# Kernel tuning notes

Hardware: AMD Instinct MI355X
Metric: run time of the kernel (lower is better)

Reference implementation:

```python
import jax, jax.numpy as jnp
import numpy as np

H = 32  # node_hidden_size
B = 16  # number of graphs in the batch


def setup_inputs() -> dict:
    key = jax.random.key(0)
    ks = iter(jax.random.split(key, 32))
    N, E = 20000, 200000
    rn = lambda s, scale=0.1: jax.random.normal(next(ks), s, dtype=jnp.float32) * scale
    return {
        "x": jax.random.normal(next(ks), (N, 4), dtype=jnp.float32),
        "edge_index": jax.random.randint(next(ks), (2, E), 0, N),
        "edge_attr": jax.random.normal(next(ks), (E,), dtype=jnp.float32),
        "batch": jnp.sort(jax.random.randint(next(ks), (N,), 0, B)),
        # project: Linear(4,32)
        "proj_w": rn((4, H)), "proj_b": jnp.zeros((H,), jnp.float32),
        # edge_nn: Linear(1,8) -> ReLU -> Linear(8,32*32)
        "e1_w": rn((1, 8)), "e1_b": jnp.zeros((8,), jnp.float32),
        "e2_w": rn((8, H * H)), "e2_b": jnp.zeros((H * H,), jnp.float32),
        # NNConv root weight + bias
        "root_w": rn((H, H)), "conv_b": jnp.zeros((H,), jnp.float32),
        # GRU(32,32), torch layout [3H, in]/[3H, H], gate order r,z,n
        "gru_wi": rn((3 * H, H)), "gru_wh": rn((3 * H, H)),
        "gru_bi": jnp.zeros((3 * H,), jnp.float32), "gru_bh": jnp.zeros((3 * H,), jnp.float32),
        # Set2Set LSTM(2H -> H), gate order i,f,g,o
        "lstm_wi": rn((4 * H, 2 * H)), "lstm_wh": rn((4 * H, H)),
        "lstm_bi": jnp.zeros((4 * H,), jnp.float32), "lstm_bh": jnp.zeros((4 * H,), jnp.float32),
        # FFN: 2H -> H -> H -> 1 (dropout is identity at inference)
        "f1_w": rn((2 * H, H)), "f1_b": jnp.zeros((H,), jnp.float32),
        "f2_w": rn((H, H)), "f2_b": jnp.zeros((H,), jnp.float32),
        "f3_w": rn((H, 1)), "f3_b": jnp.zeros((1,), jnp.float32),
    }


def reference(x, edge_index, edge_attr, batch,
              proj_w, proj_b, e1_w, e1_b, e2_w, e2_b, root_w, conv_b,
              gru_wi, gru_wh, gru_bi, gru_bh,
              lstm_wi, lstm_wh, lstm_bi, lstm_bh,
              f1_w, f1_b, f2_w, f2_b, f3_w, f3_b):
    N = x.shape[0]
    src, dst = edge_index[0], edge_index[1]

    # project node features
    h = jax.nn.relu(x @ proj_w + proj_b)              # [N, H]
    msg = h                                           # GRU hidden state

    # edge-conditioned weights (edge_attr unsqueezed to [E,1]); constant over steps
    ea = edge_attr[:, None]
    ew = (jax.nn.relu(ea @ e1_w + e1_b) @ e2_w + e2_b).reshape(-1, H, H)  # [E, in, out]

    for _ in range(3):  # message passing steps
        m = jnp.einsum('ei,eio->eo', h[src], ew)                  # per-edge matvec [E, H]
        agg = jax.ops.segment_sum(m, dst, num_segments=N)         # scatter-add to targets
        out = jax.nn.relu(agg + h @ root_w + conv_b)              # NNConv root + bias, then ReLU
        # GRU cell (seq_len=1)
        gi = out @ gru_wi.T + gru_bi
        gh = msg @ gru_wh.T + gru_bh
        r = jax.nn.sigmoid(gi[:, :H] + gh[:, :H])
        z = jax.nn.sigmoid(gi[:, H:2 * H] + gh[:, H:2 * H])
        n = jnp.tanh(gi[:, 2 * H:] + r * gh[:, 2 * H:])
        h = (1.0 - z) * n + z * msg
        msg = h

    # Set2Set readout, processing_steps=1
    q_star = jnp.zeros((B, 2 * H), x.dtype)
    hL = jnp.zeros((B, H), x.dtype)
    cL = jnp.zeros((B, H), x.dtype)
    g = q_star @ lstm_wi.T + lstm_bi + hL @ lstm_wh.T + lstm_bh   # [B, 4H]
    i_g = jax.nn.sigmoid(g[:, :H])
    f_g = jax.nn.sigmoid(g[:, H:2 * H])
    g_g = jnp.tanh(g[:, 2 * H:3 * H])
    o_g = jax.nn.sigmoid(g[:, 3 * H:])
    cL = f_g * cL + i_g * g_g
    q = o_g * jnp.tanh(cL)                                        # [B, H]
    # per-graph softmax attention
    e = jnp.sum(h * q[batch], axis=-1)                            # [N]
    e_max = jax.ops.segment_max(e, batch, num_segments=B)
    a = jnp.exp(e - e_max[batch])
    a = a / jax.ops.segment_sum(a, batch, num_segments=B)[batch]
    r_out = jax.ops.segment_sum(a[:, None] * h, batch, num_segments=B)  # [B, H]
    q_star = jnp.concatenate([q, r_out], axis=-1)                 # [B, 2H]

    # FFN (dropout = identity at inference)
    out = jax.nn.relu(q_star @ f1_w + f1_b)
    out = jax.nn.relu(out @ f2_w + f2_b)
    return out @ f3_w + f3_b                                      # [B, 1]
```

## Files before the change

kernel.cpp:

```cpp
#include <hip/hip_runtime.h>
#include <math.h>

#define H 32
#define BSEG 16
#define CHUNKS 32

__device__ __forceinline__ float sigmoidf_(float x){ return 1.f/(1.f+expf(-x)); }

__global__ __launch_bounds__(512) void k_prep(
    const float* __restrict__ gru_wi, const float* __restrict__ gru_wh,
    const float* __restrict__ gru_bi, const float* __restrict__ gru_bh,
    const float* __restrict__ lstm_bi, const float* __restrict__ lstm_bh,
    const float* __restrict__ e1w, const float* __restrict__ e1b, const float* __restrict__ e2w,
    float* __restrict__ WI, float* __restrict__ WH, float* __restrict__ BS,
    float* __restrict__ MP, float* __restrict__ MM, int* __restrict__ flag,
    float* __restrict__ qvec, unsigned int* __restrict__ segmax,
    float* __restrict__ ssum, float* __restrict__ vsum,
    int* __restrict__ cnt, int N)
{
    int t = threadIdx.x;
    for (int i = t; i < N; i += 512) cnt[i] = 0;
    for (int idx = t; idx < 3072; idx += 512) {
        int k = idx >> 10, rem = idx & 1023, i = rem >> 5, o = rem & 31;
        WI[idx] = gru_wi[(k*32 + o)*32 + i];
        WH[idx] = gru_wh[(k*32 + o)*32 + i];
    }
    for (int idx = t; idx < 1024; idx += 512) {
        float mp = 0.f, mm = 0.f;
        #pragma unroll
        for (int k = 0; k < 8; ++k) {
            float w = e1w[k];
            float v = e2w[k*1024 + idx];
            if (w > 0.f) mp = fmaf(w, v, mp);
            if (w < 0.f) mm = fmaf(w, v, mm);
        }
        MP[idx] = mp;
        MM[idx] = mm;
    }
    if (t == 0) {
        int z = 1;
        for (int k = 0; k < 8; ++k) if (e1b[k] != 0.f) z = 0;
        flag[0] = z;
    }
    if (t < 32) {
        BS[t]      = gru_bi[t]      + gru_bh[t];
        BS[32 + t] = gru_bi[32 + t] + gru_bh[32 + t];
        BS[64 + t] = gru_bi[64 + t];
        BS[96 + t] = gru_bh[64 + t];
    }
    if (t < H) {
        float g0 = lstm_bi[t] + lstm_bh[t];
        float g2 = lstm_bi[2*H + t] + lstm_bh[2*H + t];
        float g3 = lstm_bi[3*H + t] + lstm_bh[3*H + t];
        float ig = sigmoidf_(g0);
        float gg = tanhf(g2);
        float og = sigmoidf_(g3);
        qvec[t] = og * tanhf(ig * gg);
    }
    for (int i = t; i < BSEG; i += 512) { segmax[i] = 0u; ssum[i] = 0.f; }
    for (int i = t; i < BSEG*H; i += 512) vsum[i] = 0.f;
}

__global__ __launch_bounds__(256) void k_count(const int* __restrict__ ei, int* __restrict__ cnt, int E)
{
    int e = blockIdx.x * 256 + threadIdx.x;
    if (e < E) atomicAdd(&cnt[ei[E + e]], 1);
}

__global__ __launch_bounds__(1024) void k_scan(
    const int* __restrict__ cnt, int* __restrict__ rowptr, int* __restrict__ cursor, int N)
{
    __shared__ int part[1024];
    int t = threadIdx.x;
    int chunk = (N + 1023) >> 10;
    int base = t * chunk;
    int s = 0;
    for (int i = 0; i < chunk; ++i) {
        int idx = base + i;
        if (idx < N) s += cnt[idx];
    }
    part[t] = s;
    __syncthreads();
    for (int off = 1; off < 1024; off <<= 1) {
        int add = (t >= off) ? part[t - off] : 0;
        __syncthreads();
        part[t] += add;
        __syncthreads();
    }
    int run = part[t] - s;
    for (int i = 0; i < chunk; ++i) {
        int idx = base + i;
        if (idx < N) {
            rowptr[idx] = run;
            cursor[idx] = run;
            run += cnt[idx];
        }
    }
    if (t == 1023) rowptr[N] = part[1023];
}

__global__ __launch_bounds__(256) void k_scatter(
    const int* __restrict__ ei, const float* __restrict__ ea, int* __restrict__ cursor,
    int* __restrict__ esrc, float* __restrict__ eattr, int E)
{
    int e = blockIdx.x * 256 + threadIdx.x;
    if (e >= E) return;
    int dst = ei[E + e];
    int pos = atomicAdd(&cursor[dst], 1);
    esrc[pos] = ei[e];
    eattr[pos] = ea[e];
}

__device__ __forceinline__ void pass2_lds(const float* sm, int xb, int w0, int w1, int fg4,
                                          float a[4], float b[4])
{
    #pragma unroll 2
    for (int i4 = 0; i4 < 32; i4 += 4) {
        float4 xv  = *(const float4*)&sm[xb + i4];
        float4 w00 = *(const float4*)&sm[w0 + (i4+0)*32 + fg4];
        float4 w01 = *(const float4*)&sm[w0 + (i4+1)*32 + fg4];
        float4 w02 = *(const float4*)&sm[w0 + (i4+2)*32 + fg4];
        float4 w03 = *(const float4*)&sm[w0 + (i4+3)*32 + fg4];
        float4 w10 = *(const float4*)&sm[w1 + (i4+0)*32 + fg4];
        float4 w11 = *(const float4*)&sm[w1 + (i4+1)*32 + fg4];
        float4 w12 = *(const float4*)&sm[w1 + (i4+2)*32 + fg4];
        float4 w13 = *(const float4*)&sm[w1 + (i4+3)*32 + fg4];
        a[0]=fmaf(xv.x,w00.x,a[0]); a[1]=fmaf(xv.x,w00.y,a[1]); a[2]=fmaf(xv.x,w00.z,a[2]); a[3]=fmaf(xv.x,w00.w,a[3]);
        a[0]=fmaf(xv.y,w01.x,a[0]); a[1]=fmaf(xv.y,w01.y,a[1]); a[2]=fmaf(xv.y,w01.z,a[2]); a[3]=fmaf(xv.y,w01.w,a[3]);
        a[0]=fmaf(xv.z,w02.x,a[0]); a[1]=fmaf(xv.z,w02.y,a[1]); a[2]=fmaf(xv.z,w02.z,a[2]); a[3]=fmaf(xv.z,w02.w,a[3]);
        a[0]=fmaf(xv.w,w03.x,a[0]); a[1]=fmaf(xv.w,w03.y,a[1]); a[2]=fmaf(xv.w,w03.z,a[2]); a[3]=fmaf(xv.w,w03.w,a[3]);
        b[0]=fmaf(xv.x,w10.x,b[0]); b[1]=fmaf(xv.x,w10.y,b[1]); b[2]=fmaf(xv.x,w10.z,b[2]); b[3]=fmaf(xv.x,w10.w,b[3]);
        b[0]=fmaf(xv.y,w11.x,b[0]); b[1]=fmaf(xv.y,w11.y,b[1]); b[2]=fmaf(xv.y,w11.z,b[2]); b[3]=fmaf(xv.y,w11.w,b[3]);
        b[0]=fmaf(xv.z,w12.x,b[0]); b[1]=fmaf(xv.z,w12.y,b[1]); b[2]=fmaf(xv.z,w12.z,b[2]); b[3]=fmaf(xv.z,w12.w,b[3]);
        b[0]=fmaf(xv.w,w13.x,b[0]); b[1]=fmaf(xv.w,w13.y,b[1]); b[2]=fmaf(xv.w,w13.z,b[2]); b[3]=fmaf(xv.w,w13.w,b[3]);
    }
}

__device__ __forceinline__ void pass1_lds(const float* sm, int xb, int w0, int fg4, float a[4])
{
    #pragma unroll 2
    for (int i4 = 0; i4 < 32; i4 += 4) {
        float4 xv  = *(const float4*)&sm[xb + i4];
        float4 w00 = *(const float4*)&sm[w0 + (i4+0)*32 + fg4];
        float4 w01 = *(const float4*)&sm[w0 + (i4+1)*32 + fg4];
        float4 w02 = *(const float4*)&sm[w0 + (i4+2)*32 + fg4];
        float4 w03 = *(const float4*)&sm[w0 + (i4+3)*32 + fg4];
        a[0]=fmaf(xv.x,w00.x,a[0]); a[1]=fmaf(xv.x,w00.y,a[1]); a[2]=fmaf(xv.x,w00.z,a[2]); a[3]=fmaf(xv.x,w00.w,a[3]);
        a[0]=fmaf(xv.y,w01.x,a[0]); a[1]=fmaf(xv.y,w01.y,a[1]); a[2]=fmaf(xv.y,w01.z,a[2]); a[3]=fmaf(xv.y,w01.w,a[3]);
        a[0]=fmaf(xv.z,w02.x,a[0]); a[1]=fmaf(xv.z,w02.y,a[1]); a[2]=fmaf(xv.z,w02.z,a[2]); a[3]=fmaf(xv.z,w02.w,a[3]);
        a[0]=fmaf(xv.w,w03.x,a[0]); a[1]=fmaf(xv.w,w03.y,a[1]); a[2]=fmaf(xv.w,w03.z,a[2]); a[3]=fmaf(xv.w,w03.w,a[3]);
    }
}

__global__ __launch_bounds__(256) void k_proj(
    const float* __restrict__ x, const float* __restrict__ proj_w, const float* __restrict__ proj_b,
    float* __restrict__ h, int N)
{
    int n = blockIdx.x * 256 + threadIdx.x;
    if (n >= N) return;
    float4 xv = *(const float4*)&x[n * 4];
    #pragma unroll
    for (int q = 0; q < 8; ++q) {
        float r_[4];
        #pragma unroll
        for (int j = 0; j < 4; ++j) {
            int o = q*4 + j;
            float a = proj_b[o];
            a = fmaf(xv.x, proj_w[0*32 + o], a);
            a = fmaf(xv.y, proj_w[1*32 + o], a);
            a = fmaf(xv.z, proj_w[2*32 + o], a);
            a = fmaf(xv.w, proj_w[3*32 + o], a);
            r_[j] = fmaxf(a, 0.f);
        }
        *(float4*)&h[n*32 + q*4] = make_float4(r_[0], r_[1], r_[2], r_[3]);
    }
}

#define TW 3072
__global__ __launch_bounds__(256, 2) void k_tab(
    const float* __restrict__ h, const float* __restrict__ e2w, const float* __restrict__ e2b,
    const float* __restrict__ MP, const float* __restrict__ MM, const int* __restrict__ flag,
    float* __restrict__ A, int N)
{
    __shared__ float sm[TW + 4*288];
    int tid = threadIdx.x;
    int lane = tid & 63;
    int w = tid >> 6;
    int fg = lane & 7, fg4 = fg*4;
    int nw = lane >> 3;
    int n = (blockIdx.x * 4 + w) * 8 + nw;
    bool valid = (n < N);
    int nc = valid ? n : (N - 1);
    int xb = TW + w*288 + nw*36;

    float4 hv4 = *(const float4*)&h[nc*32 + fg4];
    *(float4*)&sm[xb + fg4] = hv4;

    if (flag[0]) {
        float4* s4 = (float4*)sm;
        for (int i = tid; i < 768; i += 256) {
            const float4* src = (i < 256) ? (const float4*)MP
                              : (i < 512) ? (const float4*)MM
                                          : (const float4*)e2b;
            s4[i] = src[i & 255];
        }
        __syncthreads();
        #pragma unroll 1
        for (int cc = 0; cc < 3; ++cc) {
            float acc[4] = {0.f, 0.f, 0.f, 0.f};
            pass1_lds(sm, xb, cc*1024, fg4, acc);
            if (valid)
                *(float4*)&A[(size_t)n*96 + cc*32 + fg4] =
                    make_float4(acc[0], acc[1], acc[2], acc[3]);
        }
    } else {
        #pragma unroll 1
        for (int cg = 0; cg < 3; ++cg) {
            __syncthreads();
            float4* s4 = (float4*)sm;
            for (int i = tid; i < 768; i += 256) {
                int c = cg*3 + (i >> 8);
                const float4* src = (c < 8) ? (const float4*)(e2w + (size_t)c*1024)
                                            : (const float4*)e2b;
                s4[i] = src[i & 255];
            }
            __syncthreads();
            #pragma unroll 1
            for (int cc = 0; cc < 3; ++cc) {
                float acc[4] = {0.f, 0.f, 0.f, 0.f};
                pass1_lds(sm, xb, cc*1024, fg4, acc);
                if (valid)
                    *(float4*)&A[(size_t)n*288 + (cg*3+cc)*32 + fg4] =
                        make_float4(acc[0], acc[1], acc[2], acc[3]);
            }
        }
    }
}

#define XGR 10240
__global__ __launch_bounds__(256, 2) void k_gru(
    float* __restrict__ h,
    const int* __restrict__ rowptr, const int* __restrict__ esrc, const float* __restrict__ eattr,
    const float* __restrict__ TIN, const int* __restrict__ flag,
    const float* __restrict__ root_w, const float* __restrict__ conv_b,
    const float* __restrict__ WI, const float* __restrict__ WH, const float* __restrict__ BS,
    const float* __restrict__ MP, const float* __restrict__ MM,
    const float* __restrict__ e2b, const float* __restrict__ e2w,
    const float* __restrict__ e1w, const float* __restrict__ e1b,
    float* __restrict__ TOUT, int N, int computeT)
{
    __shared__ float sm[XGR + 4*288];
    int tid = threadIdx.x;
    int fast = flag[0];
    {
        float4* s4 = (float4*)sm;
        const float4* r4  = (const float4*)root_w;
        const float4* wh4 = (const float4*)WH;
        const float4* wi4 = (const float4*)WI;
        for (int i = tid; i < 256; i += 256) s4[i] = r4[i];
        for (int i = tid; i < 768; i += 256) s4[256  + i] = wh4[i];
        for (int i = tid; i < 768; i += 256) s4[1024 + i] = wi4[i];
        if (computeT && fast) {
            for (int i = tid; i < 768; i += 256) {
                const float4* src = (i < 256) ? (const float4*)MP
                                  : (i < 512) ? (const float4*)MM
                                              : (const float4*)e2b;
                s4[1792 + i] = src[i & 255];
            }
        }
    }
    __syncthreads();

    int lane = tid & 63;
    int w = tid >> 6;
    int fg = lane & 7, fg4 = fg*4;
    int nw = lane >> 3;
    int n = (blockIdx.x * 4 + w) * 8 + nw;
    bool valid = (n < N);
    int nc = valid ? n : (N - 1);
    int xb = XGR + w*288 + nw*36;

    float4 hv4 = *(const float4*)&h[nc*32 + fg4];
    float hold[4] = {hv4.x, hv4.y, hv4.z, hv4.w};
    *(float4*)&sm[xb + fg4] = hv4;

    float av[4] = {0.f, 0.f, 0.f, 0.f};
    {
        int beg = rowptr[nc];
        int end = rowptr[nc + 1];
        if (fast) {
            for (int j = beg; j < end; ++j) {
                int src = esrc[j];
                float a = eattr[j];
                const float* base = TIN + (size_t)src * 96;
                float4 p = *(const float4*)&base[(a > 0.f ? 0 : 32) + fg4];
                float4 b = *(const float4*)&base[64 + fg4];
                av[0] += fmaf(a, p.x, b.x);
                av[1] += fmaf(a, p.y, b.y);
                av[2] += fmaf(a, p.z, b.z);
                av[3] += fmaf(a, p.w, b.w);
            }
        } else {
            for (int j = beg; j < end; ++j) {
                int src = esrc[j];
                float a = eattr[j];
                const float* Gp = TIN + (size_t)src * 288;
                float4 b = *(const float4*)&Gp[256 + fg4];
                float m0 = b.x, m1 = b.y, m2 = b.z, m3 = b.w;
                #pragma unroll
                for (int k = 0; k < 8; ++k) {
                    float t = fmaxf(fmaf(a, e1w[k], e1b[k]), 0.f);
                    float4 g = *(const float4*)&Gp[k*32 + fg4];
                    m0 = fmaf(t, g.x, m0); m1 = fmaf(t, g.y, m1);
                    m2 = fmaf(t, g.z, m2); m3 = fmaf(t, g.w, m3);
                }
                av[0] += m0; av[1] += m1; av[2] += m2; av[3] += m3;
            }
        }
    }

    float outv[4], gh2[4];
    {
        float4 cb4 = *(const float4*)&conv_b[fg4];
        outv[0]=av[0]+cb4.x; outv[1]=av[1]+cb4.y; outv[2]=av[2]+cb4.z; outv[3]=av[3]+cb4.w;
        float4 b3 = *(const float4*)&BS[96 + fg4];
        gh2[0]=b3.x; gh2[1]=b3.y; gh2[2]=b3.z; gh2[3]=b3.w;
    }
    pass2_lds(sm, xb, 0, 1024 + 2048, fg4, outv, gh2);

    float gh0[4] = {0.f,0.f,0.f,0.f};
    float gh1[4] = {0.f,0.f,0.f,0.f};
    pass2_lds(sm, xb, 1024, 2048, fg4, gh0, gh1);

    float outr[4];
    #pragma unroll
    for (int j = 0; j < 4; ++j) outr[j] = fmaxf(outv[j], 0.f);

    *(float4*)&sm[xb + fg4] = make_float4(outr[0], outr[1], outr[2], outr[3]);

    float gi0[4], gi1[4], gi2[4];
    {
        float4 b0 = *(const float4*)&BS[fg4];
        float4 b1 = *(const float4*)&BS[32 + fg4];
        float4 b2 = *(const float4*)&BS[64 + fg4];
        gi0[0]=b0.x; gi0[1]=b0.y; gi0[2]=b0.z; gi0[3]=b0.w;
        gi1[0]=b1.x; gi1[1]=b1.y; gi1[2]=b1.z; gi1[3]=b1.w;
        gi2[0]=b2.x; gi2[1]=b2.y; gi2[2]=b2.z; gi2[3]=b2.w;
    }
    pass2_lds(sm, xb, 4096, 5120, fg4, gi0, gi1);
    pass1_lds(sm, xb, 6144, fg4, gi2);

    float hnew[4];
    #pragma unroll
    for (int j = 0; j < 4; ++j) {
        float r = sigmoidf_(gi0[j] + gh0[j]);
        float z = sigmoidf_(gi1[j] + gh1[j]);
        float nn = tanhf(gi2[j] + r * gh2[j]);
        hnew[j] = (1.f - z) * nn + z * hold[j];
    }
    if (valid) *(float4*)&h[n*32 + fg4] = make_float4(hnew[0], hnew[1], hnew[2], hnew[3]);

    if (computeT) {
        *(float4*)&sm[xb + fg4] = make_float4(hnew[0], hnew[1], hnew[2], hnew[3]);
        if (fast) {
            #pragma unroll 1
            for (int cc = 0; cc < 3; ++cc) {
                float acc[4] = {0.f, 0.f, 0.f, 0.f};
                pass1_lds(sm, xb, 7168 + cc*1024, fg4, acc);
                if (valid)
                    *(float4*)&TOUT[(size_t)n*96 + cc*32 + fg4] =
                        make_float4(acc[0], acc[1], acc[2], acc[3]);
            }
        } else {
            #pragma unroll 1
            for (int cg = 0; cg < 3; ++cg) {
                __syncthreads();
                float4* s4 = (float4*)sm;
                for (int i = tid; i < 768; i += 256) {
                    int c = cg*3 + (i >> 8);
                    const float4* src = (c < 8) ? (const float4*)(e2w + (size_t)c*1024)
                                                : (const float4*)e2b;
                    s4[1792 + i] = src[i & 255];
                }
                __syncthreads();
                #pragma unroll 1
                for (int cc = 0; cc < 3; ++cc) {
                    float acc[4] = {0.f, 0.f, 0.f, 0.f};
                    pass1_lds(sm, xb, 7168 + cc*1024, fg4, acc);
                    if (valid)
                        *(float4*)&TOUT[(size_t)n*288 + (cg*3+cc)*32 + fg4] =
                            make_float4(acc[0], acc[1], acc[2], acc[3]);
                }
            }
        }
    }
}

__device__ __forceinline__ unsigned int fenc(float f) {
    int i = __float_as_int(f);
    return (i >= 0) ? ((unsigned int)i | 0x80000000u) : ~(unsigned int)i;
}
__device__ __forceinline__ float fdec(unsigned int u) {
    int i = (u & 0x80000000u) ? (int)(u & 0x7FFFFFFFu) : (int)(~u);
    return __int_as_float(i);
}

__global__ __launch_bounds__(256) void k_pass1(
    const float* __restrict__ h, const int* __restrict__ batch,
    const float* __restrict__ qvec, float* __restrict__ ebuf,
    unsigned int* __restrict__ segmax, int N)
{
    int b = blockIdx.x / CHUNKS;
    int c = blockIdx.x % CHUNKS;
    int lo = 0, hi = N;
    while (lo < hi) { int mid = (lo + hi) >> 1; if (batch[mid] < b) lo = mid + 1; else hi = mid; }
    int s = lo;
    lo = 0; hi = N;
    while (lo < hi) { int mid = (lo + hi) >> 1; if (batch[mid] < b + 1) lo = mid + 1; else hi = mid; }
    int e = lo;
    int len = e - s;
    int per = (len + CHUNKS - 1) / CHUNKS;
    int n0 = s + c * per;
    int n1 = min(n0 + per, e);

    int tid = threadIdx.x;
    int ln = tid >> 5, o = tid & 31;
    float qv = qvec[o];
    float mloc = -INFINITY;
    for (int nn = n0 + ln; nn < n1; nn += 8) {
        float v = h[nn * H + o] * qv;
        #pragma unroll
        for (int m = 16; m >= 1; m >>= 1) v += __shfl_xor(v, m);
        if (o == 0) ebuf[nn] = v;
        mloc = fmaxf(mloc, v);
    }
    __shared__ float red[256];
    red[tid] = mloc;
    __syncthreads();
    for (int st = 128; st >= 1; st >>= 1) {
        if (tid < st) red[tid] = fmaxf(red[tid], red[tid + st]);
        __syncthreads();
    }
    if (tid == 0 && n0 < n1) atomicMax(&segmax[b], fenc(red[0]));
}

__global__ __launch_bounds__(256) void k_pass2(
    const float* __restrict__ h, const int* __restrict__ batch,
    const float* __restrict__ ebuf, const unsigned int* __restrict__ segmax,
    float* __restrict__ ssum, float* __restrict__ vsum, int N)
{
    int b = blockIdx.x / CHUNKS;
    int c = blockIdx.x % CHUNKS;
    int lo = 0, hi = N;
    while (lo < hi) { int mid = (lo + hi) >> 1; if (batch[mid] < b) lo = mid + 1; else hi = mid; }
    int s = lo;
    lo = 0; hi = N;
    while (lo < hi) { int mid = (lo + hi) >> 1; if (batch[mid] < b + 1) lo = mid + 1; else hi = mid; }
    int e = lo;
    int len = e - s;
    int per = (len + CHUNKS - 1) / CHUNKS;
    int n0 = s + c * per;
    int n1 = min(n0 + per, e);

    int tid = threadIdx.x;
    int ln = tid >> 5, o = tid & 31;
    float emax = fdec(segmax[b]);
    float vacc = 0.f, sacc = 0.f;
    for (int nn = n0 + ln; nn < n1; nn += 8) {
        float a = expf(ebuf[nn] - emax);
        vacc += a * h[nn * H + o];
        if (o == 0) sacc += a;
    }
    __shared__ float vsh[8][H];
    __shared__ float ssh[8];
    vsh[ln][o] = vacc;
    if (o == 0) ssh[ln] = sacc;
    __syncthreads();
    if (tid < H) {
        float v = 0.f;
        #pragma unroll
        for (int g = 0; g < 8; ++g) v += vsh[g][tid];
        atomicAdd(&vsum[b * H + tid], v);
    } else if (tid == H) {
        float stot = 0.f;
        #pragma unroll
        for (int g = 0; g < 8; ++g) stot += ssh[g];
        atomicAdd(&ssum[b], stot);
    }
}

__global__ __launch_bounds__(512) void k_mlp(
    const float* __restrict__ qvec, const float* __restrict__ ssum, const float* __restrict__ vsum,
    const float* __restrict__ f1w, const float* __restrict__ f1b,
    const float* __restrict__ f2w, const float* __restrict__ f2b,
    const float* __restrict__ f3w, const float* __restrict__ f3b,
    float* __restrict__ out)
{
    __shared__ float qsm[BSEG][2 * H];
    __shared__ float o1[BSEG][H];
    __shared__ float o2[BSEG][H];
    int tid = threadIdx.x;
    int b = tid >> 5, j = tid & 31;
    float st = ssum[b];
    qsm[b][j] = qvec[j];
    qsm[b][H + j] = (st > 0.f) ? vsum[b * H + j] / st : 0.f;
    __syncthreads();
    float acc = f1b[j];
    for (int i = 0; i < 2 * H; ++i) acc += qsm[b][i] * f1w[i * H + j];
    o1[b][j] = fmaxf(acc, 0.f);
    __syncthreads();
    acc = f2b[j];
    for (int i = 0; i < H; ++i) acc += o1[b][i] * f2w[i * H + j];
    o2[b][j] = fmaxf(acc, 0.f);
    __syncthreads();
    float v = o2[b][j] * f3w[j];
    #pragma unroll
    for (int m = 16; m >= 1; m >>= 1) v += __shfl_xor(v, m);
    if (j == 0) out[b] = v + f3b[0];
}

extern "C" void kernel_launch(void* const* d_in, const int* in_sizes, int n_in,
                              void* d_out, int out_size, void* d_ws, size_t ws_size,
                              hipStream_t stream)
{
    const float* x      = (const float*)d_in[0];
    const int*   ei     = (const int*)d_in[1];
    const float* ea     = (const float*)d_in[2];
    const int*   batch  = (const int*)d_in[3];
    const float* proj_w = (const float*)d_in[4];
    const float* proj_b = (const float*)d_in[5];
    const float* e1w    = (const float*)d_in[6];
    const float* e1b    = (const float*)d_in[7];
    const float* e2w    = (const float*)d_in[8];
    const float* e2b    = (const float*)d_in[9];
    const float* root_w = (const float*)d_in[10];
    const float* conv_b = (const float*)d_in[11];
    const float* gru_wi = (const float*)d_in[12];
    const float* gru_wh = (const float*)d_in[13];
    const float* gru_bi = (const float*)d_in[14];
    const float* gru_bh = (const float*)d_in[15];
    const float* lstm_bi = (const float*)d_in[18];
    const float* lstm_bh = (const float*)d_in[19];
    const float* f1w    = (const float*)d_in[20];
    const float* f1b    = (const float*)d_in[21];
    const float* f2w    = (const float*)d_in[22];
    const float* f2b    = (const float*)d_in[23];
    const float* f3w    = (const float*)d_in[24];
    const float* f3b    = (const float*)d_in[25];

    const int N = in_sizes[0] / 4;
    const int E = in_sizes[2];

    float* ws   = (float*)d_ws;
    float* h    = ws;
    float* A    = h + (size_t)N * H;
    float* Bb   = A + (size_t)N * 288;
    float* ebuf = Bb + (size_t)N * 288;
    float* qvec = ebuf + N;
    unsigned int* segmax = (unsigned int*)(qvec + H);
    float* ssum = (float*)(segmax + BSEG);
    float* vsum = ssum + BSEG;
    float* WI   = vsum + BSEG * H;
    float* WH   = WI + 3072;
    float* BS   = WH + 3072;
    float* MP   = BS + 128;
    float* MM   = MP + 1024;
    int*   flag = (int*)(MM + 1024);
    int*   cnt    = flag + 1;
    int*   rowptr = cnt + N;
    int*   cursor = rowptr + N + 1;
    int*   esrc   = cursor + N;
    float* eattr  = (float*)(esrc + E);

    const int nwaves = (N + 7) / 8;
    const int nb4 = (nwaves + 3) / 4;
    const int pblocks = (N + 255) / 256;
    const int cblocks = (E + 255) / 256;

    k_prep<<<1, 512, 0, stream>>>(gru_wi, gru_wh, gru_bi, gru_bh, lstm_bi, lstm_bh,
                                  e1w, e1b, e2w,
                                  WI, WH, BS, MP, MM, flag, qvec, segmax, ssum, vsum, cnt, N);
    k_count<<<cblocks, 256, 0, stream>>>(ei, cnt, E);
    k_scan<<<1, 1024, 0, stream>>>(cnt, rowptr, cursor, N);
    k_scatter<<<cblocks, 256, 0, stream>>>(ei, ea, cursor, esrc, eattr, E);
    k_proj<<<pblocks, 256, 0, stream>>>(x, proj_w, proj_b, h, N);
    k_tab<<<nb4, 256, 0, stream>>>(h, e2w, e2b, MP, MM, flag, A, N);

    k_gru<<<nb4, 256, 0, stream>>>(h, rowptr, esrc, eattr, A, flag, root_w, conv_b,
                                   WI, WH, BS, MP, MM, e2b, e2w, e1w, e1b, Bb, N, 1);
    k_gru<<<nb4, 256, 0, stream>>>(h, rowptr, esrc, eattr, Bb, flag, root_w, conv_b,
                                   WI, WH, BS, MP, MM, e2b, e2w, e1w, e1b, A, N, 1);
    k_gru<<<nb4, 256, 0, stream>>>(h, rowptr, esrc, eattr, A, flag, root_w, conv_b,
                                   WI, WH, BS, MP, MM, e2b, e2w, e1w, e1b, Bb, N, 0);

    k_pass1<<<BSEG * CHUNKS, 256, 0, stream>>>(h, batch, qvec, ebuf, segmax, N);
    k_pass2<<<BSEG * CHUNKS, 256, 0, stream>>>(h, batch, ebuf, segmax, ssum, vsum, N);
    k_mlp<<<1, 512, 0, stream>>>(qvec, ssum, vsum, f1w, f1b, f2w, f2b, f3w, f3b, (float*)d_out);
}
```

Baseline: 191.1 us.

## Split edge aggregation into wave-per-node kernel, fuse projection and attention scores

Moves the per-node edge gather out of the GRU kernel into a new kernel where each 64-lane wave handles one node, with 8 slots striding over its incoming edges and a shuffle reduction at the end. Previously 8 lanes walked each node's edge list serially, which left degree-dependent latency inside the heavy GRU kernel. The node projection is folded into the table kernel, and the final GRU step now computes attention logits and the per-segment max, so the separate projection and pass1 kernels are removed. In exchange it adds three extra launches and an N×32 intermediate buffer that is written and read back each step.

```diff
diff --git a/kernel.cpp b/kernel.cpp
--- a/kernel.cpp
+++ b/kernel.cpp
@@ -6,6 +6,15 @@
 #define CHUNKS 32
 
 __device__ __forceinline__ float sigmoidf_(float x){ return 1.f/(1.f+expf(-x)); }
+
+__device__ __forceinline__ unsigned int fenc(float f) {
+    int i = __float_as_int(f);
+    return (i >= 0) ? ((unsigned int)i | 0x80000000u) : ~(unsigned int)i;
+}
+__device__ __forceinline__ float fdec(unsigned int u) {
+    int i = (u & 0x80000000u) ? (int)(u & 0x7FFFFFFFu) : (int)(~u);
+    return __int_as_float(i);
+}
 
 __global__ __launch_bounds__(512) void k_prep(
     const float* __restrict__ gru_wi, const float* __restrict__ gru_wh,
@@ -152,35 +161,12 @@
     }
 }
 
-__global__ __launch_bounds__(256) void k_proj(
-    const float* __restrict__ x, const float* __restrict__ proj_w, const float* __restrict__ proj_b,
-    float* __restrict__ h, int N)
-{
-    int n = blockIdx.x * 256 + threadIdx.x;
-    if (n >= N) return;
-    float4 xv = *(const float4*)&x[n * 4];
-    #pragma unroll
-    for (int q = 0; q < 8; ++q) {
-        float r_[4];
-        #pragma unroll
-        for (int j = 0; j < 4; ++j) {
-            int o = q*4 + j;
-            float a = proj_b[o];
-            a = fmaf(xv.x, proj_w[0*32 + o], a);
-            a = fmaf(xv.y, proj_w[1*32 + o], a);
-            a = fmaf(xv.z, proj_w[2*32 + o], a);
-            a = fmaf(xv.w, proj_w[3*32 + o], a);
-            r_[j] = fmaxf(a, 0.f);
-        }
-        *(float4*)&h[n*32 + q*4] = make_float4(r_[0], r_[1], r_[2], r_[3]);
-    }
-}
-
 #define TW 3072
 __global__ __launch_bounds__(256, 2) void k_tab(
-    const float* __restrict__ h, const float* __restrict__ e2w, const float* __restrict__ e2b,
+    const float* __restrict__ x, const float* __restrict__ proj_w, const float* __restrict__ proj_b,
+    const float* __restrict__ e2w, const float* __restrict__ e2b,
     const float* __restrict__ MP, const float* __restrict__ MM, const int* __restrict__ flag,
-    float* __restrict__ A, int N)
+    float* __restrict__ h, float* __restrict__ A, int N)
 {
     __shared__ float sm[TW + 4*288];
     int tid = threadIdx.x;
@@ -193,8 +179,22 @@
     int nc = valid ? n : (N - 1);
     int xb = TW + w*288 + nw*36;
 
-    float4 hv4 = *(const float4*)&h[nc*32 + fg4];
-    *(float4*)&sm[xb + fg4] = hv4;
+    {
+        float4 xv = *(const float4*)&x[nc*4];
+        float r_[4];
+        #pragma unroll
+        for (int j = 0; j < 4; ++j) {
+            int o = fg4 + j;
+            float a = proj_b[o];
+            a = fmaf(xv.x, proj_w[0*32 + o], a);
+            a = fmaf(xv.y, proj_w[1*32 + o], a);
+            a = fmaf(xv.z, proj_w[2*32 + o], a);
+            a = fmaf(xv.w, proj_w[3*32 + o], a);
+            r_[j] = fmaxf(a, 0.f);
+        }
+        if (valid) *(float4*)&h[n*32 + fg4] = make_float4(r_[0], r_[1], r_[2], r_[3]);
+        *(float4*)&sm[xb + fg4] = make_float4(r_[0], r_[1], r_[2], r_[3]);
+    }
 
     if (flag[0]) {
         float4* s4 = (float4*)sm;
@@ -237,17 +237,71 @@
     }
 }
 
+__global__ __launch_bounds__(256) void k_agg(
+    const int* __restrict__ rowptr, const int* __restrict__ esrc, const float* __restrict__ eattr,
+    const float* __restrict__ T, const int* __restrict__ flag,
+    const float* __restrict__ e1w, const float* __restrict__ e1b,
+    float* __restrict__ agg, int N)
+{
+    int n = blockIdx.x * 4 + (threadIdx.x >> 6);
+    if (n >= N) return;
+    int lane = threadIdx.x & 63;
+    int slot = lane >> 3;
+    int fg4 = (lane & 7) * 4;
+    int beg = rowptr[n];
+    int end = rowptr[n + 1];
+
+    float a0 = 0.f, a1 = 0.f, a2 = 0.f, a3 = 0.f;
+    if (flag[0]) {
+        for (int j = beg + slot; j < end; j += 8) {
+            int src = esrc[j];
+            float a = eattr[j];
+            const float* base = T + (size_t)src * 96;
+            float4 p = *(const float4*)&base[(a > 0.f ? 0 : 32) + fg4];
+            float4 b = *(const float4*)&base[64 + fg4];
+            a0 += fmaf(a, p.x, b.x);
+            a1 += fmaf(a, p.y, b.y);
+            a2 += fmaf(a, p.z, b.z);
+            a3 += fmaf(a, p.w, b.w);
+        }
+    } else {
+        for (int j = beg + slot; j < end; j += 8) {
+            int src = esrc[j];
+            float a = eattr[j];
+            const float* Gp = T + (size_t)src * 288;
+            float4 b = *(const float4*)&Gp[256 + fg4];
+            float m0 = b.x, m1 = b.y, m2 = b.z, m3 = b.w;
+            #pragma unroll
+            for (int k = 0; k < 8; ++k) {
+                float t = fmaxf(fmaf(a, e1w[k], e1b[k]), 0.f);
+                float4 g = *(const float4*)&Gp[k*32 + fg4];
+                m0 = fmaf(t, g.x, m0); m1 = fmaf(t, g.y, m1);
+                m2 = fmaf(t, g.z, m2); m3 = fmaf(t, g.w, m3);
+            }
+            a0 += m0; a1 += m1; a2 += m2; a3 += m3;
+        }
+    }
+    #pragma unroll
+    for (int m = 8; m <= 32; m <<= 1) {
+        a0 += __shfl_xor(a0, m, 64);
+        a1 += __shfl_xor(a1, m, 64);
+        a2 += __shfl_xor(a2, m, 64);
+        a3 += __shfl_xor(a3, m, 64);
+    }
+    if (slot == 0)
+        *(float4*)&agg[(size_t)n*32 + fg4] = make_float4(a0, a1, a2, a3);
+}
+
 #define XGR 10240
 __global__ __launch_bounds__(256, 2) void k_gru(
-    float* __restrict__ h,
-    const int* __restrict__ rowptr, const int* __restrict__ esrc, const float* __restrict__ eattr,
-    const float* __restrict__ TIN, const int* __restrict__ flag,
+    float* __restrict__ h, const float* __restrict__ agg, const int* __restrict__ flag,
     const float* __restrict__ root_w, const float* __restrict__ conv_b,
     const float* __restrict__ WI, const float* __restrict__ WH, const float* __restrict__ BS,
     const float* __restrict__ MP, const float* __restrict__ MM,
     const float* __restrict__ e2b, const float* __restrict__ e2w,
-    const float* __restrict__ e1w, const float* __restrict__ e1b,
-    float* __restrict__ TOUT, int N, int computeT)
+    const float* __restrict__ qvec, const int* __restrict__ batch,
+    float* __restrict__ ebuf, unsigned int* __restrict__ segmax,
+    float* __restrict__ TOUT, int N, int computeT, int computeE)
 {
     __shared__ float sm[XGR + 4*288];
     int tid = threadIdx.x;
@@ -284,45 +338,11 @@
     float hold[4] = {hv4.x, hv4.y, hv4.z, hv4.w};
     *(float4*)&sm[xb + fg4] = hv4;
 
-    float av[4] = {0.f, 0.f, 0.f, 0.f};
-    {
-        int beg = rowptr[nc];
-        int end = rowptr[nc + 1];
-        if (fast) {
-            for (int j = beg; j < end; ++j) {
-                int src = esrc[j];
-                float a = eattr[j];
-                const float* base = TIN + (size_t)src * 96;
-                float4 p = *(const float4*)&base[(a > 0.f ? 0 : 32) + fg4];
-                float4 b = *(const float4*)&base[64 + fg4];
-                av[0] += fmaf(a, p.x, b.x);
-                av[1] += fmaf(a, p.y, b.y);
-                av[2] += fmaf(a, p.z, b.z);
-                av[3] += fmaf(a, p.w, b.w);
-            }
-        } else {
-            for (int j = beg; j < end; ++j) {
-                int src = esrc[j];
-                float a = eattr[j];
-                const float* Gp = TIN + (size_t)src * 288;
-                float4 b = *(const float4*)&Gp[256 + fg4];
-                float m0 = b.x, m1 = b.y, m2 = b.z, m3 = b.w;
-                #pragma unroll
-                for (int k = 0; k < 8; ++k) {
-                    float t = fmaxf(fmaf(a, e1w[k], e1b[k]), 0.f);
-                    float4 g = *(const float4*)&Gp[k*32 + fg4];
-                    m0 = fmaf(t, g.x, m0); m1 = fmaf(t, g.y, m1);
-                    m2 = fmaf(t, g.z, m2); m3 = fmaf(t, g.w, m3);
-                }
-                av[0] += m0; av[1] += m1; av[2] += m2; av[3] += m3;
-            }
-        }
-    }
-
     float outv[4], gh2[4];
     {
+        float4 av4 = *(const float4*)&agg[(size_t)nc*32 + fg4];
         float4 cb4 = *(const float4*)&conv_b[fg4];
-        outv[0]=av[0]+cb4.x; outv[1]=av[1]+cb4.y; outv[2]=av[2]+cb4.z; outv[3]=av[3]+cb4.w;
+        outv[0]=av4.x+cb4.x; outv[1]=av4.y+cb4.y; outv[2]=av4.z+cb4.z; outv[3]=av4.w+cb4.w;
         float4 b3 = *(const float4*)&BS[96 + fg4];
         gh2[0]=b3.x; gh2[1]=b3.y; gh2[2]=b3.z; gh2[3]=b3.w;
     }
@@ -359,6 +379,18 @@
         hnew[j] = (1.f - z) * nn + z * hold[j];
     }
     if (valid) *(float4*)&h[n*32 + fg4] = make_float4(hnew[0], hnew[1], hnew[2], hnew[3]);
+
+    if (computeE) {
+        float4 qv = *(const float4*)&qvec[fg4];
+        float e = hnew[0]*qv.x + hnew[1]*qv.y + hnew[2]*qv.z + hnew[3]*qv.w;
+        e += __shfl_xor(e, 1, 64);
+        e += __shfl_xor(e, 2, 64);
+        e += __shfl_xor(e, 4, 64);
+        if (valid && fg == 0) {
+            ebuf[n] = e;
+            atomicMax(&segmax[batch[n]], fenc(e));
+        }
+    }
 
     if (computeT) {
         *(float4*)&sm[xb + fg4] = make_float4(hnew[0], hnew[1], hnew[2], hnew[3]);
@@ -396,54 +428,6 @@
     }
 }
 
-__device__ __forceinline__ unsigned int fenc(float f) {
-    int i = __float_as_int(f);
-    return (i >= 0) ? ((unsigned int)i | 0x80000000u) : ~(unsigned int)i;
-}
-__device__ __forceinline__ float fdec(unsigned int u) {
-    int i = (u & 0x80000000u) ? (int)(u & 0x7FFFFFFFu) : (int)(~u);
-    return __int_as_float(i);
-}
-
-__global__ __launch_bounds__(256) void k_pass1(
-    const float* __restrict__ h, const int* __restrict__ batch,
-    const float* __restrict__ qvec, float* __restrict__ ebuf,
-    unsigned int* __restrict__ segmax, int N)
-{
-    int b = blockIdx.x / CHUNKS;
-    int c = blockIdx.x % CHUNKS;
-    int lo = 0, hi = N;
-    while (lo < hi) { int mid = (lo + hi) >> 1; if (batch[mid] < b) lo = mid + 1; else hi = mid; }
-    int s = lo;
-    lo = 0; hi = N;
-    while (lo < hi) { int mid = (lo + hi) >> 1; if (batch[mid] < b + 1) lo = mid + 1; else hi = mid; }
-    int e = lo;
-    int len = e - s;
-    int per = (len + CHUNKS - 1) / CHUNKS;
-    int n0 = s + c * per;
-    int n1 = min(n0 + per, e);
-
-    int tid = threadIdx.x;
-    int ln = tid >> 5, o = tid & 31;
-    float qv = qvec[o];
-    float mloc = -INFINITY;
-    for (int nn = n0 + ln; nn < n1; nn += 8) {
-        float v = h[nn * H + o] * qv;
-        #pragma unroll
-        for (int m = 16; m >= 1; m >>= 1) v += __shfl_xor(v, m);
-        if (o == 0) ebuf[nn] = v;
-        mloc = fmaxf(mloc, v);
-    }
-    __shared__ float red[256];
-    red[tid] = mloc;
-    __syncthreads();
-    for (int st = 128; st >= 1; st >>= 1) {
-        if (tid < st) red[tid] = fmaxf(red[tid], red[tid + st]);
-        __syncthreads();
-    }
-    if (tid == 0 && n0 < n1) atomicMax(&segmax[b], fenc(red[0]));
-}
-
 __global__ __launch_bounds__(256) void k_pass2(
     const float* __restrict__ h, const int* __restrict__ batch,
     const float* __restrict__ ebuf, const unsigned int* __restrict__ segmax,
@@ -555,7 +539,8 @@
     float* h    = ws;
     float* A    = h + (size_t)N * H;
     float* Bb   = A + (size_t)N * 288;
-    float* ebuf = Bb + (size_t)N * 288;
+    float* agg  = Bb + (size_t)N * 288;
+    float* ebuf = agg + (size_t)N * H;
     float* qvec = ebuf + N;
     unsigned int* segmax = (unsigned int*)(qvec + H);
     float* ssum = (float*)(segmax + BSEG);
@@ -574,7 +559,7 @@
 
     const int nwaves = (N + 7) / 8;
     const int nb4 = (nwaves + 3) / 4;
-    const int pblocks = (N + 255) / 256;
+    const int ablocks = (N + 3) / 4;
     const int cblocks = (E + 255) / 256;
 
     k_prep<<<1, 512, 0, stream>>>(gru_wi, gru_wh, gru_bi, gru_bh, lstm_bi, lstm_bh,
@@ -583,17 +568,18 @@
     k_count<<<cblocks, 256, 0, stream>>>(ei, cnt, E);
     k_scan<<<1, 1024, 0, stream>>>(cnt, rowptr, cursor, N);
     k_scatter<<<cblocks, 256, 0, stream>>>(ei, ea, cursor, esrc, eattr, E);
-    k_proj<<<pblocks, 256, 0, stream>>>(x, proj_w, proj_b, h, N);
-    k_tab<<<nb4, 256, 0, stream>>>(h, e2w, e2b, MP, MM, flag, A, N);
-
-    k_gru<<<nb4, 256, 0, stream>>>(h, rowptr, esrc, eattr, A, flag, root_w, conv_b,
-                                   WI, WH, BS, MP, MM, e2b, e2w, e1w, e1b, Bb, N, 1);
-    k_gru<<<nb4, 256, 0, stream>>>(h, rowptr, esrc, eattr, Bb, flag, root_w, conv_b,
-                                   WI, WH, BS, MP, MM, e2b, e2w, e1w, e1b, A, N, 1);
-    k_gru<<<nb4, 256, 0, stream>>>(h, rowptr, esrc, eattr, A, flag, root_w, conv_b,
-                                   WI, WH, BS, MP, MM, e2b, e2w, e1w, e1b, Bb, N, 0);
-
-    k_pass1<<<BSEG * CHUNKS, 256, 0, stream>>>(h, batch, qvec, ebuf, segmax, N);
+    k_tab<<<nb4, 256, 0, stream>>>(x, proj_w, proj_b, e2w, e2b, MP, MM, flag, h, A, N);
+
+    k_agg<<<ablocks, 256, 0, stream>>>(rowptr, esrc, eattr, A, flag, e1w, e1b, agg, N);
+    k_gru<<<nb4, 256, 0, stream>>>(h, agg, flag, root_w, conv_b, WI, WH, BS, MP, MM,
+                                   e2b, e2w, qvec, batch, ebuf, segmax, Bb, N, 1, 0);
+    k_agg<<<ablocks, 256, 0, stream>>>(rowptr, esrc, eattr, Bb, flag, e1w, e1b, agg, N);
+    k_gru<<<nb4, 256, 0, stream>>>(h, agg, flag, root_w, conv_b, WI, WH, BS, MP, MM,
+                                   e2b, e2w, qvec, batch, ebuf, segmax, A, N, 1, 0);
+    k_agg<<<ablocks, 256, 0, stream>>>(rowptr, esrc, eattr, A, flag, e1w, e1b, agg, N);
+    k_gru<<<nb4, 256, 0, stream>>>(h, agg, flag, root_w, conv_b, WI, WH, BS, MP, MM,
+                                   e2b, e2w, qvec, batch, ebuf, segmax, Bb, N, 0, 1);
+
     k_pass2<<<BSEG * CHUNKS, 256, 0, stream>>>(h, batch, ebuf, segmax, ssum, vsum, N);
     k_mlp<<<1, 512, 0, stream>>>(qvec, ssum, vsum, f1w, f1b, f2w, f2b, f3w, f3b, (float*)d_out);
 }
```

After: 405.3 us. 2.12x slower.
